# Kernel optimization log

Hardware: AMD Instinct MI355X
Metric: run time of the kernel (lower is better)

Reference implementation:

```python
import jax, jax.numpy as jnp
import numpy as np
from jax import lax

B, T, I, H, O = 64, 512, 256, 1024, 1


def setup_inputs() -> dict:
    key = jax.random.key(0)
    ks = jax.random.split(key, 7)
    s_ih = 1.0 / np.sqrt(H)
    return {
        "x": jax.random.normal(ks[0], (B, T, I), dtype=jnp.float32),
        "W_ih": jax.random.uniform(ks[1], (4 * H, I), minval=-s_ih, maxval=s_ih, dtype=jnp.float32),
        "W_hh": jax.random.uniform(ks[2], (4 * H, H), minval=-s_ih, maxval=s_ih, dtype=jnp.float32),
        "b_ih": jax.random.uniform(ks[3], (4 * H,), minval=-s_ih, maxval=s_ih, dtype=jnp.float32),
        "b_hh": jax.random.uniform(ks[4], (4 * H,), minval=-s_ih, maxval=s_ih, dtype=jnp.float32),
        "fc_W": jax.random.uniform(ks[5], (O, H), minval=-s_ih, maxval=s_ih, dtype=jnp.float32),
        "fc_b": jax.random.uniform(ks[6], (O,), minval=-s_ih, maxval=s_ih, dtype=jnp.float32),
    }


def reference(x, W_ih, W_hh, b_ih, b_hh, fc_W, fc_b):
    Bd, Td, _ = x.shape
    Hd = W_hh.shape[1]
    # Precompute input projections for all timesteps: [T, B, 4H]
    x_proj = jnp.einsum('bti,gi->tbg', x, W_ih) + b_ih + b_hh

    def step(carry, xt):
        h, c = carry
        gates = xt + h @ W_hh.T  # [B, 4H]
        i_g, f_g, g_g, o_g = jnp.split(gates, 4, axis=-1)  # PyTorch order i,f,g,o
        i_g = jax.nn.sigmoid(i_g)
        f_g = jax.nn.sigmoid(f_g)
        g_g = jnp.tanh(g_g)
        o_g = jax.nn.sigmoid(o_g)
        c_new = f_g * c + i_g * g_g
        h_new = o_g * jnp.tanh(c_new)
        return (h_new, c_new), None

    h0 = jnp.zeros((Bd, Hd), dtype=x.dtype)
    c0 = jnp.zeros((Bd, Hd), dtype=x.dtype)
    (h_last, _), _ = lax.scan(step, (h0, c0), x_proj)
    out = jnp.tanh(h_last)          # tanh on last hidden state
    return out @ fc_W.T + fc_b      # [B, O]
```

## Files before the change

kernel.cpp:

```cpp
#include <hip/hip_runtime.h>
#include <hip/hip_bf16.h>


typedef __bf16 bf16_t;
typedef bf16_t b16x8 __attribute__((ext_vector_type(8)));
typedef float  f32x4 __attribute__((ext_vector_type(4)));

#define TQ 512
#define IQ 256
#define HQ 1024

#define RED(w,g,u,b) (((((w)*4 + (g))*16 + (u))*20) + (b))

union U8 { b16x8 b; unsigned long long q[2]; unsigned short u[8]; };

__device__ __forceinline__ float bf2f(unsigned short s) {
    return __uint_as_float(((unsigned)s) << 16);
}
__device__ __forceinline__ unsigned short f2bf(float f) {
    unsigned u = __float_as_uint(f);
    u += 0x7fff + ((u >> 16) & 1);
    return (unsigned short)(u >> 16);
}
__device__ __forceinline__ b16x8 cvt84(float4 a, float4 b) {
    U8 r;
    r.u[0] = f2bf(a.x); r.u[1] = f2bf(a.y); r.u[2] = f2bf(a.z); r.u[3] = f2bf(a.w);
    r.u[4] = f2bf(b.x); r.u[5] = f2bf(b.y); r.u[6] = f2bf(b.z); r.u[7] = f2bf(b.w);
    return r.b;
}
__device__ __forceinline__ b16x8 load_h16(const unsigned short* p) {
    U8 r;
    r.q[0] = __hip_atomic_load((const unsigned long long*)p,
                               __ATOMIC_RELAXED, __HIP_MEMORY_SCOPE_AGENT);
    r.q[1] = __hip_atomic_load((const unsigned long long*)(p + 4),
                               __ATOMIC_RELAXED, __HIP_MEMORY_SCOPE_AGENT);
    return r.b;
}
__device__ __forceinline__ float frcp(float x) { return __builtin_amdgcn_rcpf(x); }
__device__ __forceinline__ float sigm(float x) {
    return frcp(1.f + __expf(-x));
}
__device__ __forceinline__ float tanh_f(float v) {
    float x = fminf(fmaxf(v, -15.f), 15.f);
    float e = __expf(2.f * x);
    return (e - 1.f) * frcp(e + 1.f);
}

__launch_bounds__(512, 2)
__global__ void lstm_persist(const float* __restrict__ x,
                             const float* __restrict__ Wih,
                             const float* __restrict__ Whh,
                             const float* __restrict__ bih,
                             const float* __restrict__ bhh,
                             const float* __restrict__ fcW,
                             const float* __restrict__ fcb,
                             float* __restrict__ out,
                             unsigned short* __restrict__ hbuf,
                             unsigned int* __restrict__ bar)
{
    __shared__ float red[8 * 4 * 16 * 20];

    const int tid  = threadIdx.x;
    const int w    = tid >> 6;
    const int lane = tid & 63;
    const int bid  = blockIdx.x;
    const int bg   = bid & 3;
    const int ug   = bid >> 2;

    const int l16  = lane & 15;
    const int quad = lane >> 4;

    b16x8 wih[4];
    b16x8 whh[4][4];
    {
        const int koff = quad * 8;
        #pragma unroll
        for (int g = 0; g < 4; ++g) {
            int row = g * HQ + ug * 16 + l16;
            const float* p = Wih + (size_t)row * IQ + w * 32 + koff;
            float4 a = *(const float4*)p;
            float4 b = *(const float4*)(p + 4);
            wih[g] = cvt84(a, b);
            #pragma unroll
            for (int j = 0; j < 4; ++j) {
                int k0 = (w * 4 + j) * 32 + koff;
                const float* q = Whh + (size_t)row * HQ + k0;
                float4 c = *(const float4*)q;
                float4 e = *(const float4*)(q + 4);
                whh[j][g] = cvt84(c, e);
            }
        }
    }

    const int hi  = (lane >> 5) & 1;
    const int eb  = 2 * w + hi;
    const int dup = (lane >> 4) & 1;
    float c_st = 0.f;
    float bias_g[4];
    #pragma unroll
    for (int g = 0; g < 4; ++g) {
        int gr = g * HQ + ug * 16 + l16;
        bias_g[g] = bih[gr] + bhh[gr];
    }

    const unsigned short* hrd0 = hbuf + ((size_t)bg * 16 + l16) * HQ;
    unsigned short*       hwr0 = hbuf + (size_t)bg * 16 * HQ + (size_t)eb * HQ + ug * 16 + l16;

    const unsigned int* myfl = bar + ((size_t)(bg * 64 + w * 8 + (lane >> 3)) * 16 + (lane & 7));
    unsigned int*       wfl  = bar + ((size_t)(bg * 64 + ug) * 16 + w);

    const float* xbase = x + ((size_t)(bg * 16 + l16) * TQ) * IQ + w * 32 + quad * 8;
    float4 xa = *(const float4*)(xbase);
    float4 xb = *(const float4*)(xbase + 4);

    for (int t = 0; t < TQ; ++t) {
        const int p = t & 1;

        b16x8 ax = cvt84(xa, xb);
        f32x4 acc[4];
        #pragma unroll
        for (int g = 0; g < 4; ++g) {
            f32x4 z = {0.f, 0.f, 0.f, 0.f};
            acc[g] = __builtin_amdgcn_mfma_f32_16x16x32_bf16(ax, wih[g], z, 0, 0, 0);
        }

        const unsigned need = (unsigned)t;
        {
            unsigned v = __hip_atomic_load(myfl, __ATOMIC_RELAXED,
                                           __HIP_MEMORY_SCOPE_AGENT);
            while (!__all(v >= need))
                v = __hip_atomic_load(myfl, __ATOMIC_RELAXED,
                                      __HIP_MEMORY_SCOPE_AGENT);
        }

        const unsigned short* hread = hrd0 + (size_t)p * (4 * 16 * HQ);
        b16x8 ah[4];
        #pragma unroll
        for (int j = 0; j < 4; ++j)
            ah[j] = load_h16(hread + (w * 4 + j) * 32 + quad * 8);
        #pragma unroll
        for (int j = 0; j < 4; ++j) {
            #pragma unroll
            for (int g = 0; g < 4; ++g)
                acc[g] = __builtin_amdgcn_mfma_f32_16x16x32_bf16(ah[j], whh[j][g], acc[g], 0, 0, 0);
        }

        __syncthreads();

        #pragma unroll
        for (int g = 0; g < 4; ++g)
            *(f32x4*)&red[RED(w, g, l16, quad * 4)] = acc[g];
        __syncthreads();

        float s[4];
        #pragma unroll
        for (int g = 0; g < 4; ++g) {
            float a0 = red[RED(dup * 4 + 0, g, l16, eb)]
                     + red[RED(dup * 4 + 1, g, l16, eb)];
            float a1 = red[RED(dup * 4 + 2, g, l16, eb)]
                     + red[RED(dup * 4 + 3, g, l16, eb)];
            float as = a0 + a1;
            as += __shfl_xor(as, 16);
            s[g] = as;
        }
        {
            float gi = s[0] + bias_g[0];
            float gf = s[1] + bias_g[1];
            float gg = s[2] + bias_g[2];
            float go = s[3] + bias_g[3];
            float i_s = sigm(gi);
            float f_s = sigm(gf);
            float g_t = tanh_f(gg);
            float o_s = sigm(go);
            float c = f_s * c_st + i_s * g_t;
            c_st = c;
            float h = o_s * tanh_f(c);
            if (!dup)
                __hip_atomic_store(hwr0 + (size_t)(p ^ 1) * (4 * 16 * HQ), f2bf(h),
                                   __ATOMIC_RELAXED, __HIP_MEMORY_SCOPE_AGENT);
        }
        asm volatile("s_waitcnt vmcnt(0)" ::: "memory");
        if (lane == 0)
            __hip_atomic_store(wfl, (unsigned)(t + 1),
                               __ATOMIC_RELAXED, __HIP_MEMORY_SCOPE_AGENT);

        size_t nt = (t + 1 < TQ) ? (size_t)(t + 1) * IQ : (size_t)t * IQ;
        xa = *(const float4*)(xbase + nt);
        xb = *(const float4*)(xbase + nt + 4);
    }

    if (bid < 4) {
        #pragma unroll
        for (int pb = 0; pb < 8; ++pb) {
            const unsigned int* pf = bar + ((size_t)(bg * 64 + pb * 8 + (lane >> 3)) * 16 + (lane & 7));
            unsigned v = __hip_atomic_load(pf, __ATOMIC_RELAXED,
                                           __HIP_MEMORY_SCOPE_AGENT);
            while (!__all(v >= (unsigned)TQ))
                v = __hip_atomic_load(pf, __ATOMIC_RELAXED,
                                      __HIP_MEMORY_SCOPE_AGENT);
        }
        const unsigned short* hl = hbuf + (size_t)bg * 16 * HQ;
        float fb = fcb[0];
        #pragma unroll
        for (int r = 0; r < 2; ++r) {
            int b = w * 2 + r;
            float sacc = 0.f;
            #pragma unroll
            for (int j = 0; j < 16; ++j) {
                int u = j * 64 + lane;
                unsigned short hv = __hip_atomic_load(hl + (size_t)b * HQ + u,
                                                      __ATOMIC_RELAXED,
                                                      __HIP_MEMORY_SCOPE_AGENT);
                sacc += tanh_f(bf2f(hv)) * fcW[u];
            }
            #pragma unroll
            for (int off = 32; off > 0; off >>= 1)
                sacc += __shfl_down(sacc, off);
            if (lane == 0) out[bg * 16 + b] = sacc + fb;
        }
    }
}

extern "C" void kernel_launch(void* const* d_in, const int* in_sizes, int n_in,
                              void* d_out, int out_size, void* d_ws, size_t ws_size,
                              hipStream_t stream) {
    (void)in_sizes; (void)n_in; (void)out_size; (void)ws_size;
    const float* x   = (const float*)d_in[0];
    const float* Wih = (const float*)d_in[1];
    const float* Whh = (const float*)d_in[2];
    const float* bih = (const float*)d_in[3];
    const float* bhh = (const float*)d_in[4];
    const float* fcW = (const float*)d_in[5];
    const float* fcb = (const float*)d_in[6];
    float* out = (float*)d_out;

    unsigned short* hbuf = (unsigned short*)d_ws;
    unsigned int*   bar  = (unsigned int*)((char*)d_ws + 262144);

    hipMemsetAsync(d_ws, 0, 262144 + 16384, stream);

    void* args[] = { &x, &Wih, &Whh, &bih, &bhh, &fcW, &fcb, &out, &hbuf, &bar };
    hipLaunchCooperativeKernel(reinterpret_cast<void*>(lstm_persist),
                               dim3(256), dim3(512), args, 0, stream);
}
```

Before: 2.250 ms.

## Duplicate hidden-state and flag buffers by block parity; use sc0 sc1 vector loads

Each block now writes its hidden-state output and progress flag to two copies in the workspace. Even and odd unit-group blocks poll and read from separate copies, which halves contention on the shared cache lines during the per-timestep spin-wait and h exchange. The h read is replaced with four inline-asm dwordx4 global loads using sc0 sc1 cache bits, which bypass the caches to keep the data coherent, and a single waitcnt. The cost is double the stores per step and a larger workspace to memset. The workspace offsets are also changed.

```diff
diff --git a/kernel.cpp b/kernel.cpp
--- a/kernel.cpp
+++ b/kernel.cpp
@@ -12,7 +12,12 @@
 
 #define RED(w,g,u,b) (((((w)*4 + (g))*16 + (u))*20) + (b))
 
+#define HCOPY 131072
+#define HPBUF 65536
+#define BCOPY 4096
+
 union U8 { b16x8 b; unsigned long long q[2]; unsigned short u[8]; };
+union HU { f32x4 f; b16x8 b; };
 
 __device__ __forceinline__ float bf2f(unsigned short s) {
     return __uint_as_float(((unsigned)s) << 16);
@@ -28,14 +33,6 @@
     r.u[4] = f2bf(b.x); r.u[5] = f2bf(b.y); r.u[6] = f2bf(b.z); r.u[7] = f2bf(b.w);
     return r.b;
 }
-__device__ __forceinline__ b16x8 load_h16(const unsigned short* p) {
-    U8 r;
-    r.q[0] = __hip_atomic_load((const unsigned long long*)p,
-                               __ATOMIC_RELAXED, __HIP_MEMORY_SCOPE_AGENT);
-    r.q[1] = __hip_atomic_load((const unsigned long long*)(p + 4),
-                               __ATOMIC_RELAXED, __HIP_MEMORY_SCOPE_AGENT);
-    return r.b;
-}
 __device__ __forceinline__ float frcp(float x) { return __builtin_amdgcn_rcpf(x); }
 __device__ __forceinline__ float sigm(float x) {
     return frcp(1.f + __expf(-x));
@@ -44,6 +41,20 @@
     float x = fminf(fmaxf(v, -15.f), 15.f);
     float e = __expf(2.f * x);
     return (e - 1.f) * frcp(e + 1.f);
+}
+
+__device__ __forceinline__ void load_h64_sys(b16x8* ah, const unsigned short* p0) {
+    HU h0, h1, h2, h3;
+    asm volatile(
+        "global_load_dwordx4 %0, %4, off sc0 sc1\n\t"
+        "global_load_dwordx4 %1, %4, off offset:64 sc0 sc1\n\t"
+        "global_load_dwordx4 %2, %4, off offset:128 sc0 sc1\n\t"
+        "global_load_dwordx4 %3, %4, off offset:192 sc0 sc1\n\t"
+        "s_waitcnt vmcnt(0)"
+        : "=&v"(h0.f), "=&v"(h1.f), "=&v"(h2.f), "=&v"(h3.f)
+        : "v"(p0)
+        : "memory");
+    ah[0] = h0.b; ah[1] = h1.b; ah[2] = h2.b; ah[3] = h3.b;
 }
 
 __launch_bounds__(512, 2)
@@ -66,6 +77,7 @@
     const int bid  = blockIdx.x;
     const int bg   = bid & 3;
     const int ug   = bid >> 2;
+    const int par  = ug & 1;
 
     const int l16  = lane & 15;
     const int quad = lane >> 4;
@@ -103,11 +115,14 @@
         bias_g[g] = bih[gr] + bhh[gr];
     }
 
-    const unsigned short* hrd0 = hbuf + ((size_t)bg * 16 + l16) * HQ;
-    unsigned short*       hwr0 = hbuf + (size_t)bg * 16 * HQ + (size_t)eb * HQ + ug * 16 + l16;
-
-    const unsigned int* myfl = bar + ((size_t)(bg * 64 + w * 8 + (lane >> 3)) * 16 + (lane & 7));
-    unsigned int*       wfl  = bar + ((size_t)(bg * 64 + ug) * 16 + w);
+    const unsigned short* hrd0 = hbuf + (size_t)par * HCOPY
+                               + ((size_t)bg * 16 + l16) * HQ + w * 128 + quad * 8;
+    unsigned short* hwr0 = hbuf + (size_t)bg * 16 * HQ + (size_t)eb * HQ + ug * 16 + l16;
+
+    const unsigned int* myfl = bar + (size_t)par * BCOPY
+                             + ((size_t)(bg * 64 + w * 8 + (lane >> 3)) * 16 + (lane & 7));
+    unsigned int* wfl0 = bar + ((size_t)(bg * 64 + ug) * 16 + w);
+    unsigned int* wfl1 = wfl0 + BCOPY;
 
     const float* xbase = x + ((size_t)(bg * 16 + l16) * TQ) * IQ + w * 32 + quad * 8;
     float4 xa = *(const float4*)(xbase);
@@ -133,11 +148,8 @@
                                       __HIP_MEMORY_SCOPE_AGENT);
         }
 
-        const unsigned short* hread = hrd0 + (size_t)p * (4 * 16 * HQ);
         b16x8 ah[4];
-        #pragma unroll
-        for (int j = 0; j < 4; ++j)
-            ah[j] = load_h16(hread + (w * 4 + j) * 32 + quad * 8);
+        load_h64_sys(ah, hrd0 + (size_t)p * HPBUF);
         #pragma unroll
         for (int j = 0; j < 4; ++j) {
             #pragma unroll
@@ -175,14 +187,21 @@
             float c = f_s * c_st + i_s * g_t;
             c_st = c;
             float h = o_s * tanh_f(c);
-            if (!dup)
-                __hip_atomic_store(hwr0 + (size_t)(p ^ 1) * (4 * 16 * HQ), f2bf(h),
+            if (!dup) {
+                unsigned short hv = f2bf(h);
+                __hip_atomic_store(hwr0 + (size_t)(p ^ 1) * HPBUF, hv,
                                    __ATOMIC_RELAXED, __HIP_MEMORY_SCOPE_AGENT);
+                __hip_atomic_store(hwr0 + HCOPY + (size_t)(p ^ 1) * HPBUF, hv,
+                                   __ATOMIC_RELAXED, __HIP_MEMORY_SCOPE_AGENT);
+            }
         }
         asm volatile("s_waitcnt vmcnt(0)" ::: "memory");
-        if (lane == 0)
-            __hip_atomic_store(wfl, (unsigned)(t + 1),
+        if (lane == 0) {
+            __hip_atomic_store(wfl0, (unsigned)(t + 1),
                                __ATOMIC_RELAXED, __HIP_MEMORY_SCOPE_AGENT);
+            __hip_atomic_store(wfl1, (unsigned)(t + 1),
+                               __ATOMIC_RELAXED, __HIP_MEMORY_SCOPE_AGENT);
+        }
 
         size_t nt = (t + 1 < TQ) ? (size_t)(t + 1) * IQ : (size_t)t * IQ;
         xa = *(const float4*)(xbase + nt);
@@ -235,9 +254,9 @@
     float* out = (float*)d_out;
 
     unsigned short* hbuf = (unsigned short*)d_ws;
-    unsigned int*   bar  = (unsigned int*)((char*)d_ws + 262144);
-
-    hipMemsetAsync(d_ws, 0, 262144 + 16384, stream);
+    unsigned int*   bar  = (unsigned int*)((char*)d_ws + 524288);
+
+    hipMemsetAsync(d_ws, 0, 524288 + 32768, stream);
 
     void* args[] = { &x, &Wih, &Whh, &bih, &bhh, &fcW, &fcb, &out, &hbuf, &bar };
     hipLaunchCooperativeKernel(reinterpret_cast<void*>(lstm_persist),
```

Result: faster. 2.100 ms (-6.7%).
